# Performance work log

Measured on AMD Instinct MI355X. Metric: run time of the kernel, lower is better.

## Reference

```python
import jax, jax.numpy as jnp
import numpy as np

B, S, D, H = 4, 2048, 1024, 16
DH = D // H
NEG = -1e6  # d2l masked_softmax fill value


def setup_inputs() -> dict:
    key = jax.random.key(0)
    kq, kk, kv, kl, k1, k2, k3, k4 = jax.random.split(key, 8)
    scale = 1.0 / np.sqrt(D)
    return {
        "queries": jax.random.normal(kq, (B, S, D), jnp.float32),
        "keys": jax.random.normal(kk, (B, S, D), jnp.float32),
        "values": jax.random.normal(kv, (B, S, D), jnp.float32),
        "valid_lens": jax.random.randint(kl, (B,), 1, S + 1, jnp.int32),
        "W_q": jax.random.normal(k1, (D, D), jnp.float32) * scale,
        "W_k": jax.random.normal(k2, (D, D), jnp.float32) * scale,
        "W_v": jax.random.normal(k3, (D, D), jnp.float32) * scale,
        "W_o": jax.random.normal(k4, (D, D), jnp.float32) * scale,
    }


def reference(queries, keys, values, valid_lens, W_q, W_k, W_v, W_o):
    # Linear projections (bias=False); torch Linear stores W as (out, in): y = x @ W.T
    def split_heads(x):  # (B,S,D) -> (B,H,S,DH)
        return x.reshape(B, S, H, DH).transpose(0, 2, 1, 3)

    q = split_heads(queries @ W_q.T)
    k = split_heads(keys @ W_k.T)
    v = split_heads(values @ W_v.T)

    scores = jnp.einsum("bhqd,bhkd->bhqk", q, k) / jnp.sqrt(jnp.float32(DH))
    # masked_softmax: mask key positions >= valid_len (per batch; repeat over heads == broadcast)
    key_mask = jnp.arange(S)[None, :] < valid_lens[:, None]  # (B,S)
    scores = jnp.where(key_mask[:, None, None, :], scores, NEG)
    attn = jax.nn.softmax(scores, axis=-1)
    out = jnp.einsum("bhqk,bhkd->bhqd", attn, v)
    out = out.transpose(0, 2, 1, 3).reshape(B, S, D)  # concat heads
    return out @ W_o.T
```

## Files before the change

kernel.cpp:

```cpp
#include <hip/hip_runtime.h>
#include <math.h>

#define BB 4
#define SS 2048
#define DD 1024
#define HH 16
#define DHH 64
#define NBH 64
#define SCC 0.18033688011112042f

typedef __attribute__((ext_vector_type(8))) short bf16x8;
typedef __attribute__((ext_vector_type(8))) unsigned short ushort8;
typedef __attribute__((ext_vector_type(4))) float f32x4;
typedef __attribute__((ext_vector_type(16))) float f32x16;
typedef __attribute__((ext_vector_type(2))) unsigned u32x2;
typedef unsigned short u16;

__device__ inline u16 f2bf(float x) {
    union { float f; unsigned u; } v; v.f = x;
    unsigned r = v.u + 0x7fffu + ((v.u >> 16) & 1u);
    return (u16)(r >> 16);
}

__device__ inline void gload16(const u16* g, u16* l) {
    __builtin_amdgcn_global_load_lds(
        (const __attribute__((address_space(1))) unsigned int*)(const void*)g,
        (__attribute__((address_space(3))) unsigned int*)(void*)l, 16, 0, 0);
}

__device__ inline void plswap(unsigned& a, unsigned& b) {
    u32x2 r = __builtin_amdgcn_permlane32_swap(a, b, false, false);
    a = r[0]; b = r[1];
}
__device__ inline float xhalf_max(float x) {
    u32x2 r = __builtin_amdgcn_permlane32_swap(
        __float_as_uint(x), __float_as_uint(x), false, false);
    return fmaxf(__uint_as_float(r[0]), __uint_as_float(r[1]));
}
__device__ inline float xhalf_sum(float x) {
    u32x2 r = __builtin_amdgcn_permlane32_swap(
        __float_as_uint(x), __float_as_uint(x), false, false);
    return __uint_as_float(r[0]) + __uint_as_float(r[1]);
}

__global__ __launch_bounds__(256)
void cvt_all(const float* __restrict__ q, const float* __restrict__ k,
             const float* __restrict__ v,
             const float* __restrict__ wq, const float* __restrict__ wk,
             const float* __restrict__ wv, const float* __restrict__ wo,
             const int* __restrict__ vlens,
             u16* __restrict__ oq, u16* __restrict__ ok, u16* __restrict__ ov,
             u16* __restrict__ owq, u16* __restrict__ owk,
             u16* __restrict__ owv, u16* __restrict__ owo)
{
    const int id = blockIdx.x;
    const float* s; u16* d; size_t i0;
    if (id < 12288) {
        const int y = id >> 12, xx = id & 4095;
        i0 = (size_t)xx * 2048;
        if (y == 0) { s = q; d = oq; }
        else if (y == 1) { s = k; d = ok; }
        else { s = v; d = ov; }
        if (y != 0) {
            const int b  = (int)(i0 >> 21);
            const int s0 = (int)(i0 >> 10) & (SS - 1);
            const int c32 = ((vlens[b] + 31) >> 5) << 5;
            if (s0 >= c32) return;
        }
    } else {
        const int r = id - 12288;
        const int y = r >> 9, xx = r & 511;
        i0 = (size_t)xx * 2048;
        if (y == 0) { s = wq; d = owq; }
        else if (y == 1) { s = wk; d = owk; }
        else if (y == 2) { s = wv; d = owv; }
        else { s = wo; d = owo; }
    }
    const size_t i = i0 + (size_t)threadIdx.x * 8;
    const float4 a = *(const float4*)(s + i);
    const float4 c = *(const float4*)(s + i + 4);
    ushort8 r;
    r[0] = f2bf(a.x); r[1] = f2bf(a.y); r[2] = f2bf(a.z); r[3] = f2bf(a.w);
    r[4] = f2bf(c.x); r[5] = f2bf(c.y); r[6] = f2bf(c.z); r[7] = f2bf(c.w);
    *(ushort8*)(d + i) = r;
}

__global__ __launch_bounds__(256)
void transpose_v(const u16* __restrict__ Vp, const int* __restrict__ vlens,
                 u16* __restrict__ Vt)
{
    __shared__ __align__(16) u16 tile[64][72];
    const int t = threadIdx.x;
    const int s0 = blockIdx.x * 64;
    const int bh = blockIdx.y;
    const int b  = bh >> 4;
    const int c32 = ((vlens[b] + 31) >> 5) << 5;
    if (s0 >= c32) return;
    const u16* src = Vp + ((size_t)bh * SS + s0) * DHH;
    const int r = t >> 2, d0 = (t & 3) * 16;
    *(ushort8*)&tile[r][d0]     = *(const ushort8*)(src + r * DHH + d0);
    *(ushort8*)&tile[r][d0 + 8] = *(const ushort8*)(src + r * DHH + d0 + 8);
    __syncthreads();
    const int d = t >> 2, sl = (t & 3) * 16;
    ushort8 o0, o1;
    #pragma unroll
    for (int j = 0; j < 8; ++j) o0[j] = tile[sl + j][d];
    #pragma unroll
    for (int j = 0; j < 8; ++j) o1[j] = tile[sl + 8 + j][d];
    u16* dst = Vt + ((size_t)bh * DHH + d) * SS + s0 + sl;
    *(ushort8*)dst       = o0;
    *(ushort8*)(dst + 8) = o1;
}

template<int OUT_MODE>
__device__ __forceinline__
void gemm_core(const u16* __restrict__ A, const u16* __restrict__ B,
               void* __restrict__ Cv, int m0, int n0, u16* As, u16* Bs)
{
    const int t = threadIdx.x;
    const int w = t >> 6, l = t & 63;
    const int lm = l & 15, lg = l >> 4;
    const int wr = w >> 1, wc = w & 1;

    const u16* ga = A + (size_t)(m0 + w * 32 + (l >> 2)) * DD + (l & 3) * 8;
    const u16* gb = B + (size_t)(n0 + w * 32 + (l >> 2)) * DD + (l & 3) * 8;
    u16* lA0 = &As[w * 1024];
    u16* lA1 = &As[w * 1024 + 512];
    u16* lB0 = &Bs[w * 1024];
    u16* lB1 = &Bs[w * 1024 + 512];

    f32x4 acc[4][4];
    #pragma unroll
    for (int i = 0; i < 4; ++i)
        #pragma unroll
        for (int j = 0; j < 4; ++j)
            acc[i][j] = (f32x4){0.f, 0.f, 0.f, 0.f};

    for (int k0 = 0; k0 < DD; k0 += 32) {
        __syncthreads();
        gload16(ga + k0,           lA0);
        gload16(ga + k0 + 16 * DD, lA1);
        gload16(gb + k0,           lB0);
        gload16(gb + k0 + 16 * DD, lB1);
        __syncthreads();
        bf16x8 af[4], bfr[4];
        #pragma unroll
        for (int mi = 0; mi < 4; ++mi)
            af[mi] = *(const bf16x8*)&As[(wr * 64 + mi * 16 + lm) * 32 + lg * 8];
        #pragma unroll
        for (int ni = 0; ni < 4; ++ni)
            bfr[ni] = *(const bf16x8*)&Bs[(wc * 64 + ni * 16 + lm) * 32 + lg * 8];
        #pragma unroll
        for (int mi = 0; mi < 4; ++mi)
            #pragma unroll
            for (int ni = 0; ni < 4; ++ni)
                acc[mi][ni] = __builtin_amdgcn_mfma_f32_16x16x32_bf16(
                    af[mi], bfr[ni], acc[mi][ni], 0, 0, 0);
    }

    #pragma unroll
    for (int mi = 0; mi < 4; ++mi) {
        #pragma unroll
        for (int r = 0; r < 4; ++r) {
            const int m = m0 + wr * 64 + mi * 16 + lg * 4 + r;
            if (OUT_MODE == 0) {
                float* C = (float*)Cv;
                #pragma unroll
                for (int ni = 0; ni < 4; ++ni)
                    C[(size_t)m * DD + n0 + wc * 64 + ni * 16 + lm] = acc[mi][ni][r];
            } else {
                u16* C = (u16*)Cv;
                const int b = m >> 11, s = m & (SS - 1);
                #pragma unroll
                for (int ni = 0; ni < 4; ++ni) {
                    const int n = n0 + wc * 64 + ni * 16 + lm;
                    const int h = n >> 6, dh = n & 63;
                    C[(((size_t)b * HH + h) * SS + s) * DHH + dh] = f2bf(acc[mi][ni][r]);
                }
            }
        }
    }
}

__global__ __launch_bounds__(256)
void gemm_qkv(const u16* __restrict__ Xq, const u16* __restrict__ Xk,
              const u16* __restrict__ Xv,
              const u16* __restrict__ Wqb, const u16* __restrict__ Wkb,
              const u16* __restrict__ Wvb,
              u16* __restrict__ Qo, u16* __restrict__ Ko, u16* __restrict__ Vo,
              const int* __restrict__ vlens)
{
    __shared__ __align__(16) u16 As[128 * 32];
    __shared__ __align__(16) u16 Bs[128 * 32];
    const int z = blockIdx.z;
    const int m0 = blockIdx.y * 128, n0 = blockIdx.x * 128;
    const u16* A; const u16* B; u16* C;
    if (z == 0) { A = Xq; B = Wqb; C = Qo; }
    else if (z == 1) { A = Xk; B = Wkb; C = Ko; }
    else { A = Xv; B = Wvb; C = Vo; }
    if (z != 0) {
        const int b = m0 >> 11, s0 = m0 & (SS - 1);
        const int c32 = ((vlens[b] + 31) >> 5) << 5;
        if (s0 >= c32) return;
    }
    gemm_core<1>(A, B, (void*)C, m0, n0, As, Bs);
}

__global__ __launch_bounds__(256)
void gemm_out(const u16* __restrict__ A, const u16* __restrict__ B,
              float* __restrict__ C)
{
    __shared__ __align__(16) u16 As[128 * 32];
    __shared__ __align__(16) u16 Bs[128 * 32];
    gemm_core<0>(A, B, (void*)C, blockIdx.y * 128, blockIdx.x * 128, As, Bs);
}

#define LOADK4(coff) do {                                                      \
    const u16* kp_ = kb + (size_t)(coff) * DHH;                                \
    kf[0] = *(const bf16x8*)kp_;                                               \
    kf[1] = *(const bf16x8*)(kp_ + 16);                                        \
    kf[2] = *(const bf16x8*)(kp_ + 32);                                        \
    kf[3] = *(const bf16x8*)(kp_ + 48);                                        \
} while (0)

#define LOADV4(coff) do {                                                      \
    const u16* vp_ = vb + (coff);                                              \
    va[0] = *(const bf16x8*)vp_;                                               \
    va[1] = *(const bf16x8*)(vp_ + 16);                                        \
    va[2] = *(const bf16x8*)(vp_ + (size_t)32 * SS);                           \
    va[3] = *(const bf16x8*)(vp_ + (size_t)32 * SS + 16);                      \
} while (0)

__global__ __launch_bounds__(64, 2)
void flash_mfma13(const u16* __restrict__ Qp, const u16* __restrict__ Kp,
                  const u16* __restrict__ Vt, const int* __restrict__ vlens,
                  u16* __restrict__ AO)
{
    const int l = threadIdx.x;
    const int l31 = l & 31, hi = l >> 5;
    const int x = blockIdx.x;
    const int xcd = x & 7;
    const int idx = x >> 3;
    const int bh  = xcd + ((idx >> 5) << 3);
    const int qpair = idx & 31;
    const int b = bh >> 4, h = bh & 15;
    const int q0 = qpair * 64;
    const int vlen = vlens[b];
    const int ntb = (vlen + 31) >> 5;

    const u16* qbA = Qp + ((size_t)bh * SS + q0 + l31) * DHH + hi * 8;
    bf16x8 qvA[4], qvB[4];
    qvA[0] = *(const bf16x8*)qbA;
    qvA[1] = *(const bf16x8*)(qbA + 16);
    qvA[2] = *(const bf16x8*)(qbA + 32);
    qvA[3] = *(const bf16x8*)(qbA + 48);
    const u16* qbB = qbA + (size_t)32 * DHH;
    qvB[0] = *(const bf16x8*)qbB;
    qvB[1] = *(const bf16x8*)(qbB + 16);
    qvB[2] = *(const bf16x8*)(qbB + 32);
    qvB[3] = *(const bf16x8*)(qbB + 48);

    const u16* kb = Kp + ((size_t)bh * SS + l31) * DHH + hi * 8;
    const u16* vb = Vt + ((size_t)bh * DHH + l31) * SS + hi * 8;

    bf16x8 kf[4], va[4];
    LOADK4(0);
    LOADV4(0);

    f32x16 oA0, oA1, oB0, oB1;
    #pragma unroll
    for (int r = 0; r < 16; ++r) { oA0[r] = 0.f; oA1[r] = 0.f; oB0[r] = 0.f; oB1[r] = 0.f; }
    float mA = -3e38f, lA = 0.f, mB = -3e38f, lB = 0.f;

    for (int tt = 0; tt < ntb; ++tt) {
        const int c0 = tt * 32;
        f32x16 zA, zB;
        #pragma unroll
        for (int r = 0; r < 16; ++r) { zA[r] = 0.f; zB[r] = 0.f; }
        __builtin_amdgcn_s_setprio(1);
        zA = __builtin_amdgcn_mfma_f32_32x32x16_bf16(kf[0], qvA[0], zA, 0, 0, 0);
        zB = __builtin_amdgcn_mfma_f32_32x32x16_bf16(kf[0], qvB[0], zB, 0, 0, 0);
        zA = __builtin_amdgcn_mfma_f32_32x32x16_bf16(kf[1], qvA[1], zA, 0, 0, 0);
        zB = __builtin_amdgcn_mfma_f32_32x32x16_bf16(kf[1], qvB[1], zB, 0, 0, 0);
        zA = __builtin_amdgcn_mfma_f32_32x32x16_bf16(kf[2], qvA[2], zA, 0, 0, 0);
        zB = __builtin_amdgcn_mfma_f32_32x32x16_bf16(kf[2], qvB[2], zB, 0, 0, 0);
        zA = __builtin_amdgcn_mfma_f32_32x32x16_bf16(kf[3], qvA[3], zA, 0, 0, 0);
        zB = __builtin_amdgcn_mfma_f32_32x32x16_bf16(kf[3], qvB[3], zB, 0, 0, 0);
        __builtin_amdgcn_s_setprio(0);
        if (tt + 1 < ntb) LOADK4(c0 + 32);

        if (vlen - c0 < 32) {
            #pragma unroll
            for (int r = 0; r < 16; ++r) {
                const int kvl = (r & 3) + 8 * (r >> 2) + 4 * hi;
                if (c0 + kvl >= vlen) { zA[r] = -3e38f; zB[r] = -3e38f; }
            }
        }

        float mxA = fmaxf(zA[0], zA[1]);
        float mxB = fmaxf(zB[0], zB[1]);
        #pragma unroll
        for (int r = 2; r < 16; ++r) { mxA = fmaxf(mxA, zA[r]); mxB = fmaxf(mxB, zB[r]); }
        mxA = xhalf_max(mxA);
        mxB = xhalf_max(mxB);

        float corrA = 1.f, corrB = 1.f;
        if (!__all(mxA <= mA + 64.0f)) {
            const float mold = mA;
            mA = fmaxf(mA, mxA);
            corrA = exp2f((mold - mA) * SCC);
            #pragma unroll
            for (int r = 0; r < 16; ++r) { oA0[r] *= corrA; oA1[r] *= corrA; }
        }
        if (!__all(mxB <= mB + 64.0f)) {
            const float mold = mB;
            mB = fmaxf(mB, mxB);
            corrB = exp2f((mold - mB) * SCC);
            #pragma unroll
            for (int r = 0; r < 16; ++r) { oB0[r] *= corrB; oB1[r] *= corrB; }
        }

        const float mscA = mA * SCC, mscB = mB * SCC;
        float tsA = 0.f, tsB = 0.f;
        #pragma unroll
        for (int r = 0; r < 16; ++r) {
            const float pA = exp2f(__builtin_fmaf(zA[r], SCC, -mscA));
            const float pB = exp2f(__builtin_fmaf(zB[r], SCC, -mscB));
            zA[r] = pA; zB[r] = pB;
            tsA += pA; tsB += pB;
        }
        tsA = xhalf_sum(tsA);
        tsB = xhalf_sum(tsB);
        lA = lA * corrA + tsA;
        lB = lB * corrB + tsB;

        unsigned a0, a1, a2, a3, a4, a5, a6, a7;
        unsigned b0, b1, b2, b3, b4, b5, b6, b7;
        asm("v_cvt_pk_bf16_f32 %0, %1, %2" : "=v"(a0) : "v"(zA[0]),  "v"(zA[1]));
        asm("v_cvt_pk_bf16_f32 %0, %1, %2" : "=v"(a1) : "v"(zA[2]),  "v"(zA[3]));
        asm("v_cvt_pk_bf16_f32 %0, %1, %2" : "=v"(a2) : "v"(zA[4]),  "v"(zA[5]));
        asm("v_cvt_pk_bf16_f32 %0, %1, %2" : "=v"(a3) : "v"(zA[6]),  "v"(zA[7]));
        asm("v_cvt_pk_bf16_f32 %0, %1, %2" : "=v"(a4) : "v"(zA[8]),  "v"(zA[9]));
        asm("v_cvt_pk_bf16_f32 %0, %1, %2" : "=v"(a5) : "v"(zA[10]), "v"(zA[11]));
        asm("v_cvt_pk_bf16_f32 %0, %1, %2" : "=v"(a6) : "v"(zA[12]), "v"(zA[13]));
        asm("v_cvt_pk_bf16_f32 %0, %1, %2" : "=v"(a7) : "v"(zA[14]), "v"(zA[15]));
        asm("v_cvt_pk_bf16_f32 %0, %1, %2" : "=v"(b0) : "v"(zB[0]),  "v"(zB[1]));
        asm("v_cvt_pk_bf16_f32 %0, %1, %2" : "=v"(b1) : "v"(zB[2]),  "v"(zB[3]));
        asm("v_cvt_pk_bf16_f32 %0, %1, %2" : "=v"(b2) : "v"(zB[4]),  "v"(zB[5]));
        asm("v_cvt_pk_bf16_f32 %0, %1, %2" : "=v"(b3) : "v"(zB[6]),  "v"(zB[7]));
        asm("v_cvt_pk_bf16_f32 %0, %1, %2" : "=v"(b4) : "v"(zB[8]),  "v"(zB[9]));
        asm("v_cvt_pk_bf16_f32 %0, %1, %2" : "=v"(b5) : "v"(zB[10]), "v"(zB[11]));
        asm("v_cvt_pk_bf16_f32 %0, %1, %2" : "=v"(b6) : "v"(zB[12]), "v"(zB[13]));
        asm("v_cvt_pk_bf16_f32 %0, %1, %2" : "=v"(b7) : "v"(zB[14]), "v"(zB[15]));

        plswap(a0, a2); plswap(a1, a3); plswap(a4, a6); plswap(a5, a7);
        plswap(b0, b2); plswap(b1, b3); plswap(b4, b6); plswap(b5, b7);

        bf16x8 pA0, pA1, pB0, pB1;
        ((unsigned*)&pA0)[0] = a0; ((unsigned*)&pA0)[1] = a1;
        ((unsigned*)&pA0)[2] = a2; ((unsigned*)&pA0)[3] = a3;
        ((unsigned*)&pA1)[0] = a4; ((unsigned*)&pA1)[1] = a5;
        ((unsigned*)&pA1)[2] = a6; ((unsigned*)&pA1)[3] = a7;
        ((unsigned*)&pB0)[0] = b0; ((unsigned*)&pB0)[1] = b1;
        ((unsigned*)&pB0)[2] = b2; ((unsigned*)&pB0)[3] = b3;
        ((unsigned*)&pB1)[0] = b4; ((unsigned*)&pB1)[1] = b5;
        ((unsigned*)&pB1)[2] = b6; ((unsigned*)&pB1)[3] = b7;

        __builtin_amdgcn_s_setprio(1);
        oA0 = __builtin_amdgcn_mfma_f32_32x32x16_bf16(va[0], pA0, oA0, 0, 0, 0);
        oB0 = __builtin_amdgcn_mfma_f32_32x32x16_bf16(va[0], pB0, oB0, 0, 0, 0);
        oA1 = __builtin_amdgcn_mfma_f32_32x32x16_bf16(va[2], pA0, oA1, 0, 0, 0);
        oB1 = __builtin_amdgcn_mfma_f32_32x32x16_bf16(va[2], pB0, oB1, 0, 0, 0);
        oA0 = __builtin_amdgcn_mfma_f32_32x32x16_bf16(va[1], pA1, oA0, 0, 0, 0);
        oB0 = __builtin_amdgcn_mfma_f32_32x32x16_bf16(va[1], pB1, oB0, 0, 0, 0);
        oA1 = __builtin_amdgcn_mfma_f32_32x32x16_bf16(va[3], pA1, oA1, 0, 0, 0);
        oB1 = __builtin_amdgcn_mfma_f32_32x32x16_bf16(va[3], pB1, oB1, 0, 0, 0);
        __builtin_amdgcn_s_setprio(0);
        if (tt + 1 < ntb) LOADV4(c0 + 32);
    }

    const float invA = 1.f / lA;
    const float invB = 1.f / lB;
    u16* obA = AO + ((size_t)b * SS + q0 + l31) * DD + h * DHH + hi * 4;
    u16* obB = obA + (size_t)32 * DD;
    #pragma unroll
    for (int rq = 0; rq < 4; ++rq) {
        #pragma unroll
        for (int rp = 0; rp < 2; ++rp) {
            const int r = rq * 4 + rp * 2;
            unsigned w0, w1, w2, w3;
            asm("v_cvt_pk_bf16_f32 %0, %1, %2" : "=v"(w0)
                : "v"(oA0[r] * invA), "v"(oA0[r + 1] * invA));
            asm("v_cvt_pk_bf16_f32 %0, %1, %2" : "=v"(w1)
                : "v"(oA1[r] * invA), "v"(oA1[r + 1] * invA));
            asm("v_cvt_pk_bf16_f32 %0, %1, %2" : "=v"(w2)
                : "v"(oB0[r] * invB), "v"(oB0[r + 1] * invB));
            asm("v_cvt_pk_bf16_f32 %0, %1, %2" : "=v"(w3)
                : "v"(oB1[r] * invB), "v"(oB1[r + 1] * invB));
            *(unsigned*)(obA + rq * 8 + rp * 2)      = w0;
            *(unsigned*)(obA + 32 + rq * 8 + rp * 2) = w1;
            *(unsigned*)(obB + rq * 8 + rp * 2)      = w2;
            *(unsigned*)(obB + 32 + rq * 8 + rp * 2) = w3;
        }
    }
}

extern "C" void kernel_launch(void* const* d_in, const int* in_sizes, int n_in,
                              void* d_out, int out_size, void* d_ws, size_t ws_size,
                              hipStream_t stream) {
    const float* queries = (const float*)d_in[0];
    const float* keys    = (const float*)d_in[1];
    const float* values  = (const float*)d_in[2];
    const int*   vlens   = (const int*)d_in[3];
    const float* Wq      = (const float*)d_in[4];
    const float* Wk      = (const float*)d_in[5];
    const float* Wv      = (const float*)d_in[6];
    const float* Wo      = (const float*)d_in[7];

    u16* ws = (u16*)d_ws;
    const size_t NX = (size_t)BB * SS * DD;
    const size_t NW = (size_t)DD * DD;
    u16* Xq  = ws;
    u16* Xk  = Xq  + NX;
    u16* Xv  = Xk  + NX;
    u16* Wqb = Xv  + NX;
    u16* Wkb = Wqb + NW;
    u16* Wvb = Wkb + NW;
    u16* Wob = Wvb + NW;
    u16* Qp  = Wob + NW;
    u16* Kp  = Qp  + NX;
    u16* Vp  = Kp  + NX;
    u16* Vtb = Vp  + NX;
    u16* AO  = Xq;

    cvt_all<<<dim3(14336), 256, 0, stream>>>(queries, keys, values,
                                             Wq, Wk, Wv, Wo, vlens,
                                             Xq, Xk, Xv, Wqb, Wkb, Wvb, Wob);

    gemm_qkv<<<dim3(DD / 128, (BB * SS) / 128, 3), 256, 0, stream>>>(
        Xq, Xk, Xv, Wqb, Wkb, Wvb, Qp, Kp, Vp, vlens);

    transpose_v<<<dim3(SS / 64, NBH), 256, 0, stream>>>(Vp, vlens, Vtb);
    flash_mfma13<<<dim3(2048), 64, 0, stream>>>(Qp, Kp, Vtb, vlens, AO);

    gemm_out<<<dim3(DD / 128, (BB * SS) / 128), 256, 0, stream>>>(AO, Wob, (float*)d_out);
}
```

Baseline: 205.9 us.

## Split long key ranges across two flash blocks and merge partials

For batches whose valid length exceeds half the sequence, the attention kernel now launches two blocks per query tile, each handling half of the key tiles. Each block writes a bf16 partial output plus its running max and sum, and a new combine kernel rescales and merges the two halves. This balances work across batches with uneven valid lengths and raises occupancy (launch bounds 4). The cost is an extra kernel launch, extra global traffic for the partial outputs, and a second bf16 rounding of the partial results.

```diff
diff --git a/kernel.cpp b/kernel.cpp
--- a/kernel.cpp
+++ b/kernel.cpp
@@ -20,6 +20,10 @@
     union { float f; unsigned u; } v; v.f = x;
     unsigned r = v.u + 0x7fffu + ((v.u >> 16) & 1u);
     return (u16)(r >> 16);
+}
+__device__ inline float bf2f(u16 x) {
+    union { unsigned u; float f; } v; v.u = ((unsigned)x) << 16;
+    return v.f;
 }
 
 __device__ inline void gload16(const u16* g, u16* l) {
@@ -231,22 +235,30 @@
     va[3] = *(const bf16x8*)(vp_ + (size_t)32 * SS + 16);                      \
 } while (0)
 
-__global__ __launch_bounds__(64, 2)
-void flash_mfma13(const u16* __restrict__ Qp, const u16* __restrict__ Kp,
+__global__ __launch_bounds__(64, 4)
+void flash_mfma14(const u16* __restrict__ Qp, const u16* __restrict__ Kp,
                   const u16* __restrict__ Vt, const int* __restrict__ vlens,
-                  u16* __restrict__ AO)
+                  u16* __restrict__ AO, u16* __restrict__ Op1,
+                  float2* __restrict__ Mlp)
 {
     const int l = threadIdx.x;
     const int l31 = l & 31, hi = l >> 5;
     const int x = blockIdx.x;
-    const int xcd = x & 7;
-    const int idx = x >> 3;
-    const int bh  = xcd + ((idx >> 5) << 3);
+    const int xcd  = x & 7;
+    const int rest = x >> 3;
+    const int half = rest & 1;
+    const int idx  = rest >> 1;
+    const int bh   = xcd + ((idx >> 5) << 3);
     const int qpair = idx & 31;
     const int b = bh >> 4, h = bh & 15;
     const int q0 = qpair * 64;
     const int vlen = vlens[b];
-    const int ntb = (vlen + 31) >> 5;
+    const int split = vlen > 1024;
+    if (!split && half) return;
+    const int ntb  = (vlen + 31) >> 5;
+    const int ntb2 = (ntb + 1) >> 1;
+    const int tb0 = split ? (half ? ntb2 : 0) : 0;
+    const int tb1 = split ? (half ? ntb : ntb2) : ntb;
 
     const u16* qbA = Qp + ((size_t)bh * SS + q0 + l31) * DHH + hi * 8;
     bf16x8 qvA[4], qvB[4];
@@ -264,15 +276,15 @@
     const u16* vb = Vt + ((size_t)bh * DHH + l31) * SS + hi * 8;
 
     bf16x8 kf[4], va[4];
-    LOADK4(0);
-    LOADV4(0);
+    LOADK4(tb0 * 32);
+    LOADV4(tb0 * 32);
 
     f32x16 oA0, oA1, oB0, oB1;
     #pragma unroll
     for (int r = 0; r < 16; ++r) { oA0[r] = 0.f; oA1[r] = 0.f; oB0[r] = 0.f; oB1[r] = 0.f; }
     float mA = -3e38f, lA = 0.f, mB = -3e38f, lB = 0.f;
 
-    for (int tt = 0; tt < ntb; ++tt) {
+    for (int tt = tb0; tt < tb1; ++tt) {
         const int c0 = tt * 32;
         f32x16 zA, zB;
         #pragma unroll
@@ -287,7 +299,7 @@
         zA = __builtin_amdgcn_mfma_f32_32x32x16_bf16(kf[3], qvA[3], zA, 0, 0, 0);
         zB = __builtin_amdgcn_mfma_f32_32x32x16_bf16(kf[3], qvB[3], zB, 0, 0, 0);
         __builtin_amdgcn_s_setprio(0);
-        if (tt + 1 < ntb) LOADK4(c0 + 32);
+        if (tt + 1 < tb1) LOADK4(c0 + 32);
 
         if (vlen - c0 < 32) {
             #pragma unroll
@@ -376,13 +388,20 @@
         oA1 = __builtin_amdgcn_mfma_f32_32x32x16_bf16(va[3], pA1, oA1, 0, 0, 0);
         oB1 = __builtin_amdgcn_mfma_f32_32x32x16_bf16(va[3], pB1, oB1, 0, 0, 0);
         __builtin_amdgcn_s_setprio(0);
-        if (tt + 1 < ntb) LOADV4(c0 + 32);
+        if (tt + 1 < tb1) LOADV4(c0 + 32);
     }
 
     const float invA = 1.f / lA;
     const float invB = 1.f / lB;
-    u16* obA = AO + ((size_t)b * SS + q0 + l31) * DD + h * DHH + hi * 4;
+    u16* base = (split && half) ? Op1 : AO;
+    u16* obA = base + ((size_t)b * SS + q0 + l31) * DD + h * DHH + hi * 4;
     u16* obB = obA + (size_t)32 * DD;
+    if (split && hi == 0) {
+        float2 mlA; mlA.x = mA; mlA.y = lA;
+        float2 mlB; mlB.x = mB; mlB.y = lB;
+        Mlp[(size_t)half * NBH * SS + (size_t)bh * SS + q0 + l31]      = mlA;
+        Mlp[(size_t)half * NBH * SS + (size_t)bh * SS + q0 + 32 + l31] = mlB;
+    }
     #pragma unroll
     for (int rq = 0; rq < 4; ++rq) {
         #pragma unroll
@@ -405,6 +424,38 @@
     }
 }
 
+__global__ __launch_bounds__(256)
+void combine_halves(const int* __restrict__ vlens,
+                    const float2* __restrict__ Mlp,
+                    const u16* __restrict__ Op1, u16* __restrict__ AO)
+{
+    const int tid = blockIdx.x * 256 + threadIdx.x;
+    const int h = tid & 15;
+    const int rowq = tid >> 4;
+    const int b = rowq >> 11, q = rowq & 2047;
+    if (vlens[b] <= 1024) return;
+    const int bh = b * 16 + h;
+    const float2 ml0 = Mlp[(size_t)bh * SS + q];
+    const float2 ml1 = Mlp[(size_t)NBH * SS + (size_t)bh * SS + q];
+    const float M  = fmaxf(ml0.x, ml1.x);
+    const float e0 = exp2f((ml0.x - M) * SCC) * ml0.y;
+    const float e1 = exp2f((ml1.x - M) * SCC) * ml1.y;
+    const float inv = 1.f / (e0 + e1);
+    const float a0 = e0 * inv, a1 = e1 * inv;
+    u16* ao = AO + ((size_t)b * SS + q) * DD + h * DHH;
+    const u16* p1 = Op1 + ((size_t)b * SS + q) * DD + h * DHH;
+    #pragma unroll
+    for (int i = 0; i < 8; ++i) {
+        const ushort8 x0 = *(const ushort8*)(ao + i * 8);
+        const ushort8 x1 = *(const ushort8*)(p1 + i * 8);
+        ushort8 o;
+        #pragma unroll
+        for (int j = 0; j < 8; ++j)
+            o[j] = f2bf(a0 * bf2f(x0[j]) + a1 * bf2f(x1[j]));
+        *(ushort8*)(ao + i * 8) = o;
+    }
+}
+
 extern "C" void kernel_launch(void* const* d_in, const int* in_sizes, int n_in,
                               void* d_out, int out_size, void* d_ws, size_t ws_size,
                               hipStream_t stream) {
@@ -432,6 +483,8 @@
     u16* Vp  = Kp  + NX;
     u16* Vtb = Vp  + NX;
     u16* AO  = Xq;
+    u16* Op1 = Xk;
+    float2* Mlp = (float2*)Xv;
 
     cvt_all<<<dim3(14336), 256, 0, stream>>>(queries, keys, values,
                                              Wq, Wk, Wv, Wo, vlens,
@@ -441,7 +494,8 @@
         Xq, Xk, Xv, Wqb, Wkb, Wvb, Qp, Kp, Vp, vlens);
 
     transpose_v<<<dim3(SS / 64, NBH), 256, 0, stream>>>(Vp, vlens, Vtb);
-    flash_mfma13<<<dim3(2048), 64, 0, stream>>>(Qp, Kp, Vtb, vlens, AO);
+    flash_mfma14<<<dim3(4096), 64, 0, stream>>>(Qp, Kp, Vtb, vlens, AO, Op1, Mlp);
+    combine_halves<<<dim3(512), 256, 0, stream>>>(vlens, Mlp, Op1, AO);
 
     gemm_out<<<dim3(DD / 128, (BB * SS) / 128), 256, 0, stream>>>(AO, Wob, (float*)d_out);
 }
```

New measurement: 440.2 us. 2.14x slower.

## Double GEMM K-tile to 64 with XOR-swizzled shared memory layout

Applied to the files above, without the earlier changes.

The projection and output GEMMs now stage 64-wide K slices per iteration instead of 32, which halves the number of barrier pairs per K loop. Shared tiles grow to 128x64 per operand. An XOR swizzle on the 16-byte column chunk, applied on both the global-to-LDS copy and the fragment reads, is meant to avoid LDS bank conflicts with the wider rows. The trade-off is double the LDS footprint per block, which may reduce occupancy.

```diff
diff --git a/kernel.cpp b/kernel.cpp
--- a/kernel.cpp
+++ b/kernel.cpp
@@ -122,12 +122,12 @@
     const int lm = l & 15, lg = l >> 4;
     const int wr = w >> 1, wc = w & 1;
 
-    const u16* ga = A + (size_t)(m0 + w * 32 + (l >> 2)) * DD + (l & 3) * 8;
-    const u16* gb = B + (size_t)(n0 + w * 32 + (l >> 2)) * DD + (l & 3) * 8;
-    u16* lA0 = &As[w * 1024];
-    u16* lA1 = &As[w * 1024 + 512];
-    u16* lB0 = &Bs[w * 1024];
-    u16* lB1 = &Bs[w * 1024 + 512];
+    const int lrow = l >> 3;
+    const int lcb  = (l & 7) ^ lrow;
+    const u16* ga = A + (size_t)(m0 + w * 32 + lrow) * DD + lcb * 8;
+    const u16* gb = B + (size_t)(n0 + w * 32 + lrow) * DD + lcb * 8;
+    u16* lA = &As[w * 2048];
+    u16* lB = &Bs[w * 2048];
 
     f32x4 acc[4][4];
     #pragma unroll
@@ -136,26 +136,37 @@
         for (int j = 0; j < 4; ++j)
             acc[i][j] = (f32x4){0.f, 0.f, 0.f, 0.f};
 
-    for (int k0 = 0; k0 < DD; k0 += 32) {
+    for (int k0 = 0; k0 < DD; k0 += 64) {
         __syncthreads();
-        gload16(ga + k0,           lA0);
-        gload16(ga + k0 + 16 * DD, lA1);
-        gload16(gb + k0,           lB0);
-        gload16(gb + k0 + 16 * DD, lB1);
+        gload16(ga + k0,           lA);
+        gload16(ga + k0 +  8 * DD, lA + 512);
+        gload16(ga + k0 + 16 * DD, lA + 1024);
+        gload16(ga + k0 + 24 * DD, lA + 1536);
+        gload16(gb + k0,           lB);
+        gload16(gb + k0 +  8 * DD, lB + 512);
+        gload16(gb + k0 + 16 * DD, lB + 1024);
+        gload16(gb + k0 + 24 * DD, lB + 1536);
         __syncthreads();
-        bf16x8 af[4], bfr[4];
-        #pragma unroll
-        for (int mi = 0; mi < 4; ++mi)
-            af[mi] = *(const bf16x8*)&As[(wr * 64 + mi * 16 + lm) * 32 + lg * 8];
-        #pragma unroll
-        for (int ni = 0; ni < 4; ++ni)
-            bfr[ni] = *(const bf16x8*)&Bs[(wc * 64 + ni * 16 + lm) * 32 + lg * 8];
-        #pragma unroll
-        for (int mi = 0; mi < 4; ++mi)
-            #pragma unroll
-            for (int ni = 0; ni < 4; ++ni)
-                acc[mi][ni] = __builtin_amdgcn_mfma_f32_16x16x32_bf16(
-                    af[mi], bfr[ni], acc[mi][ni], 0, 0, 0);
+        #pragma unroll
+        for (int kk = 0; kk < 2; ++kk) {
+            bf16x8 af[4], bfr[4];
+            #pragma unroll
+            for (int mi = 0; mi < 4; ++mi) {
+                const int R = wr * 64 + mi * 16 + lm;
+                af[mi] = *(const bf16x8*)&As[R * 64 + (((kk * 4 + lg) ^ (R & 7)) * 8)];
+            }
+            #pragma unroll
+            for (int ni = 0; ni < 4; ++ni) {
+                const int R = wc * 64 + ni * 16 + lm;
+                bfr[ni] = *(const bf16x8*)&Bs[R * 64 + (((kk * 4 + lg) ^ (R & 7)) * 8)];
+            }
+            #pragma unroll
+            for (int mi = 0; mi < 4; ++mi)
+                #pragma unroll
+                for (int ni = 0; ni < 4; ++ni)
+                    acc[mi][ni] = __builtin_amdgcn_mfma_f32_16x16x32_bf16(
+                        af[mi], bfr[ni], acc[mi][ni], 0, 0, 0);
+        }
     }
 
     #pragma unroll
@@ -190,8 +201,8 @@
               u16* __restrict__ Qo, u16* __restrict__ Ko, u16* __restrict__ Vo,
               const int* __restrict__ vlens)
 {
-    __shared__ __align__(16) u16 As[128 * 32];
-    __shared__ __align__(16) u16 Bs[128 * 32];
+    __shared__ __align__(16) u16 As[128 * 64];
+    __shared__ __align__(16) u16 Bs[128 * 64];
     const int z = blockIdx.z;
     const int m0 = blockIdx.y * 128, n0 = blockIdx.x * 128;
     const u16* A; const u16* B; u16* C;
@@ -210,8 +221,8 @@
 void gemm_out(const u16* __restrict__ A, const u16* __restrict__ B,
               float* __restrict__ C)
 {
-    __shared__ __align__(16) u16 As[128 * 32];
-    __shared__ __align__(16) u16 Bs[128 * 32];
+    __shared__ __align__(16) u16 As[128 * 64];
+    __shared__ __align__(16) u16 Bs[128 * 64];
     gemm_core<0>(A, B, (void*)C, blockIdx.y * 128, blockIdx.x * 128, As, Bs);
 }
 
```

After: 191.9 us, median of 2. -6.8%, faster.
